# Kernel tuning notes

Measured on AMD Instinct MI355X. Metric: run time of the kernel, lower is better.

Reference implementation:

```python
import jax, jax.numpy as jnp
import numpy as np

B_SZ = 32; CTX = 8192; NP = 512; P = 16          # batch, context, n_patches, patch_size
DM = 1024; DS = 16; DC = 4; EXP = 2               # d_model, d_state, d_conv, expand
DI = EXP * DM                                     # d_inner = 2048
DTR = DM // 16                                    # dt_rank = 64


def _ln(x, g, b, eps=1e-5):
    m = x.mean(-1, keepdims=True)
    v = ((x - m) ** 2).mean(-1, keepdims=True)
    return (x - m) / jnp.sqrt(v + eps) * g + b


def _posemb_sincos_1d(n, d, temperature=10000.0):
    pos = jnp.arange(n, dtype=jnp.float32)
    omega = jnp.arange(d // 2, dtype=jnp.float32) / (d // 2 - 1)
    omega = 1.0 / (temperature ** omega)
    ang = pos[:, None] * omega[None, :]            # [n, d/2]
    return jnp.concatenate([jnp.sin(ang), jnp.cos(ang)], axis=1)  # [n, d]


def setup_inputs() -> dict:
    key = jax.random.key(0)
    ks = jax.random.split(key, 10)
    s = lambda k, shape, scale: jax.random.normal(k, shape, jnp.float32) * scale
    return {
        "x": jax.random.normal(ks[0], (B_SZ, CTX), jnp.float32),
        # patch embedding: LN(patch) -> Linear(P, DM) -> LN(DM)
        "ln1_g": jnp.ones((P,), jnp.float32), "ln1_b": jnp.zeros((P,), jnp.float32),
        "Wp": s(ks[1], (P, DM), P ** -0.5), "bp": jnp.zeros((DM,), jnp.float32),
        "ln2_g": jnp.ones((DM,), jnp.float32), "ln2_b": jnp.zeros((DM,), jnp.float32),
        # Mamba block params (mamba-ssm conventions: in_proj/out_proj bias=False, conv bias=True)
        "W_in": s(ks[2], (DM, 2 * DI), DM ** -0.5),
        "conv_w": s(ks[3], (DI, DC), DC ** -0.5), "conv_b": jnp.zeros((DI,), jnp.float32),
        "W_x": s(ks[4], (DI, DTR + 2 * DS), DI ** -0.5),
        "W_dt": s(ks[5], (DTR, DI), DTR ** -0.5),
        "b_dt": jnp.full((DI,), -4.6, jnp.float32),  # softplus(b_dt) ~ 0.01 (typical dt init)
        "A_log": jnp.log(jnp.broadcast_to(jnp.arange(1, DS + 1, dtype=jnp.float32), (DI, DS))),
        "D": jnp.ones((DI,), jnp.float32),
        "W_out": s(ks[6], (DI, DM), DI ** -0.5),
        "ln3_g": jnp.ones((DM,), jnp.float32), "ln3_b": jnp.zeros((DM,), jnp.float32),
        "Wh": s(ks[7], (DM, 1), DM ** -0.5), "bh": jnp.zeros((1,), jnp.float32),
    }


def reference(x, ln1_g, ln1_b, Wp, bp, ln2_g, ln2_b, W_in, conv_w, conv_b,
              W_x, W_dt, b_dt, A_log, D, W_out, ln3_g, ln3_b, Wh, bh):
    B = x.shape[0]
    # --- patch embedding: 'b 1 (n p) -> b n p' (c=1), LN, Linear, LN ---
    patches = x.reshape(B, NP, P)
    h = _ln(patches, ln1_g, ln1_b)
    h = h @ Wp + bp
    h = _ln(h, ln2_g, ln2_b)                        # [B, NP, DM]
    h = h + _posemb_sincos_1d(NP, DM)
    # --- Mamba block ---
    xz = h @ W_in                                   # [B, NP, 2*DI]
    u, z = jnp.split(xz, 2, axis=-1)                # [B, NP, DI] each
    # causal depthwise conv1d (kernel DC, left-padded), then SiLU
    up = jnp.pad(u, ((0, 0), (DC - 1, 0), (0, 0)))
    uc = sum(up[:, k:k + NP, :] * conv_w[:, k] for k in range(DC)) + conv_b
    uc = jax.nn.silu(uc)
    # input-dependent SSM params
    xd = uc @ W_x                                   # [B, NP, DTR+2*DS]
    dt, Bm, Cm = jnp.split(xd, [DTR, DTR + DS], axis=-1)
    delta = jax.nn.softplus(dt @ W_dt + b_dt)       # [B, NP, DI]
    A = -jnp.exp(A_log)                             # [DI, DS]

    def step(hstate, inps):
        d_t, B_t, C_t, u_t = inps                   # [B,DI], [B,DS], [B,DS], [B,DI]
        dA = jnp.exp(d_t[..., None] * A)            # [B, DI, DS]
        hstate = hstate * dA + (d_t * u_t)[..., None] * B_t[:, None, :]
        y_t = jnp.einsum('bdn,bn->bd', hstate, C_t)
        return hstate, y_t

    h0 = jnp.zeros((B, DI, DS), x.dtype)
    xs = (delta.transpose(1, 0, 2), Bm.transpose(1, 0, 2),
          Cm.transpose(1, 0, 2), uc.transpose(1, 0, 2))
    _, ys = jax.lax.scan(step, h0, xs)              # ys: [NP, B, DI]
    y = ys.transpose(1, 0, 2) + uc * D              # skip connection D*u
    y = y * jax.nn.silu(z)                          # gate
    y = y @ W_out                                   # [B, NP, DM]
    pooled = y.mean(axis=1)                         # [B, DM]
    out = (_ln(pooled, ln3_g, ln3_b) @ Wh + bh).squeeze()  # [B]
    return out
```

## Files before the change

kernel.cpp:

```cpp
#include <hip/hip_runtime.h>
#include <hip/hip_bf16.h>

#define BSZ  32
#define CTX  8192
#define NP_  512
#define PSZ  16
#define DM_  1024
#define DS_  16
#define DI_  2048
#define DTR_ 64
#define NTOK (BSZ*NP_)

typedef __hip_bfloat16 bf16;
typedef short bf16x8 __attribute__((ext_vector_type(8)));
typedef float f32x4  __attribute__((ext_vector_type(4)));

typedef __attribute__((address_space(3))) void lds_t;
typedef __attribute__((address_space(1))) void gbl_t;

__device__ inline float bf2f(bf16 v){ return __bfloat162float(v); }
__device__ inline bf16  f2bf(float v){ return __float2bfloat16(v); }
__device__ inline float bfs2f(short s){ union{unsigned u; float f;} x; x.u = ((unsigned)(unsigned short)s)<<16; return x.f; }
__device__ inline short f2bfs(float v){ bf16 b = f2bf(v); return *reinterpret_cast<short*>(&b); }
__device__ inline float fast_sigmoid(float x){ return 1.0f/(1.0f+__expf(-x)); }
__device__ inline void stout(float* p, float v){ *p = v; }
__device__ inline void stout(bf16* p, float v){ *p = f2bf(v); }
__device__ inline float hw_exp2(float x){ float r; asm("v_exp_f32 %0, %1" : "=v"(r) : "v"(x)); return r; }
__device__ inline float hw_log2(float x){ float r; asm("v_log_f32 %0, %1" : "=v"(r) : "v"(x)); return r; }
__device__ inline float softplus_fast(float x){
  if (x > 15.0f) return x;
  return 0.69314718f * hw_log2(1.0f + hw_exp2(x * 1.44269504f));
}

__device__ inline void gload_lds16(const void* g, void* l){
  __builtin_amdgcn_global_load_lds((const gbl_t*)g, (lds_t*)l, 16, 0, 0);
}

__device__ inline void transpose_cvt_body(
    int bx, int by, const float* __restrict__ W, bf16* __restrict__ T,
    int ldw, int col0, int nvalid, int K, int tid, float (*tile)[65])
{
  int kb = bx << 6, nb = by << 6;
  int c = tid & 63, r4 = tid >> 6;
  #pragma unroll
  for (int i=0;i<16;i++){
    int r = r4 + i*4;
    int kk = kb + r, nn = nb + c;
    float v = 0.f;
    if (kk < K && nn < nvalid) v = W[(size_t)kk*ldw + col0 + nn];
    tile[r][c] = v;
  }
  __syncthreads();
  #pragma unroll
  for (int i=0;i<16;i++){
    int r = r4 + i*4;
    T[(size_t)(nb + r)*K + kb + c] = f2bf(tile[c][r]);
  }
}

__global__ __launch_bounds__(256) void k_prep_all(
    const float* __restrict__ W_in, bf16* __restrict__ winT,
    const float* __restrict__ W_x,  bf16* __restrict__ wxT,
    const float* __restrict__ W_dt, bf16* __restrict__ wdtT,
    float* __restrict__ pe,
    const float* __restrict__ cw, float* __restrict__ cwT)
{
  __shared__ float tile[64][65];
  int b = blockIdx.x, tid = threadIdx.x;
  if (b < 1024){
    transpose_cvt_body(b & 15, b >> 4, W_in, winT, 4096, 0, 4096, 1024, tid, tile);
  } else if (b < 1088){
    int t = b - 1024;
    transpose_cvt_body(t & 31, t >> 5, W_x, wxT, 96, 0, 96, 2048, tid, tile);
  } else if (b < 1120){
    int t = b - 1088;
    transpose_cvt_body(0, t, W_dt, wdtT, 2048, 0, 2048, 64, tid, tile);
  } else if (b < 3168){
    int idx = (b - 1120)*256 + tid;
    int n = idx >> 10, c = idx & 1023;
    int j2 = c & 511;
    float omega = exp2f(-13.2877123795495f * ((float)j2 * (1.0f/511.0f)));
    float ang = (float)n * omega;
    pe[idx] = (c < 512) ? sinf(ang) : cosf(ang);
  } else {
    int idx = (b - 3168)*256 + tid;
    int k = idx >> 11, d = idx & 2047;
    cwT[idx] = cw[d*4 + k];
  }
}

__global__ __launch_bounds__(256) void k_patch(
    const float* __restrict__ x, const float* __restrict__ g1, const float* __restrict__ b1,
    const float* __restrict__ Wp, const float* __restrict__ bp,
    const float* __restrict__ g2, const float* __restrict__ b2,
    const float* __restrict__ pe, bf16* __restrict__ h)
{
  __shared__ float pns[2][16];
  __shared__ float red[8];
  int tid = threadIdx.x;
  int w = tid >> 6, l = tid & 63;
  int tok0 = blockIdx.x << 4;
  int bb = tok0 >> 9, n0 = tok0 & 511;
  float wreg[4][16];
  #pragma unroll
  for (int q=0;q<4;q++)
    #pragma unroll
    for (int i=0;i<16;i++)
      wreg[q][i] = Wp[i*1024 + tid + q*256];
  float bpv[4], g2v[4], b2v[4];
  #pragma unroll
  for (int q=0;q<4;q++){
    int j = tid + q*256;
    bpv[q] = bp[j]; g2v[q] = g2[j]; b2v[q] = b2[j];
  }
  float g1v = 0.f, b1v = 0.f;
  if (tid < 16){ g1v = g1[tid]; b1v = b1[tid]; }
  for (int tt=0; tt<16; ++tt){
    int buf = tt & 1;
    if (tid < 16){
      float v = x[(size_t)bb*CTX + (n0+tt)*16 + tid];
      float m = v;
      #pragma unroll
      for (int o=1;o<16;o<<=1) m += __shfl_xor(m, o, 64);
      m *= (1.0f/16.0f);
      float dv = v - m;
      float s = dv*dv;
      #pragma unroll
      for (int o=1;o<16;o<<=1) s += __shfl_xor(s, o, 64);
      float rs = rsqrtf(s*(1.0f/16.0f) + 1e-5f);
      pns[buf][tid] = dv*rs*g1v + b1v;
    }
    __syncthreads();
    float acc[4];
    #pragma unroll
    for (int q=0;q<4;q++) acc[q] = bpv[q];
    #pragma unroll
    for (int i=0;i<16;i++){
      float p = pns[buf][i];
      #pragma unroll
      for (int q=0;q<4;q++) acc[q] += p*wreg[q][i];
    }
    float s1 = acc[0]+acc[1]+acc[2]+acc[3];
    float s2 = acc[0]*acc[0]+acc[1]*acc[1]+acc[2]*acc[2]+acc[3]*acc[3];
    #pragma unroll
    for (int o=32;o;o>>=1){ s1 += __shfl_down(s1,o,64); s2 += __shfl_down(s2,o,64); }
    if (l==0){ red[w]=s1; red[4+w]=s2; }
    __syncthreads();
    float mu  = (red[0]+red[1]+red[2]+red[3])*(1.0f/1024.0f);
    float var = (red[4]+red[5]+red[6]+red[7])*(1.0f/1024.0f) - mu*mu;
    float rs2 = rsqrtf(var + 1e-5f);
    size_t tok = (size_t)(tok0 + tt);
    #pragma unroll
    for (int q=0;q<4;q++){
      int j = tid + q*256;
      float val = (acc[q]-mu)*rs2*g2v[q] + b2v[q] + pe[(n0+tt)*1024 + j];
      h[tok*1024 + j] = f2bf(val);
    }
  }
}

__global__ __launch_bounds__(512, 2) void k_gemm256(
    const bf16* __restrict__ A, const bf16* __restrict__ BT,
    bf16* __restrict__ Cu, bf16* __restrict__ Cz, int M, int N, int K)
{
  __shared__ __align__(16) bf16 As[2][256*64];
  __shared__ __align__(16) bf16 Bs[2][256*64];
  const int tid = threadIdx.x;
  const int w = tid >> 6, l = tid & 63, lr = l & 15, lg = l >> 4;
  const int wm = w >> 2, wn = w & 3;
  int nblk = N >> 8;
  int nwg = gridDim.x;
  int wg  = (blockIdx.x & 7) * (nwg >> 3) + (blockIdx.x >> 3);
  const int GM = 4;
  int band = GM * nblk;
  int grp = wg / band, loc = wg % band;
  int bm = grp*GM + (loc % GM);
  int bn = loc / GM;
  int m0 = bm << 8, n0 = bn << 8;

  f32x4 acc[8][4] = {};

  int rowS[4], colS[4];
  #pragma unroll
  for (int j=0;j<4;j++){
    int bo = (j*8 + w)*1024 + l*16;
    int r = bo >> 7;
    int c = (bo & 127) ^ ((r & 7) << 4);
    rowS[j] = r; colS[j] = c >> 1;
  }
  const bf16* Ag = A  + (size_t)m0 * K;
  const bf16* Bg = BT + (size_t)n0 * K;

  #define STAGE(buf, kt) do {                                                   \
    _Pragma("unroll")                                                           \
    for (int j=0;j<4;j++)                                                       \
      gload_lds16(Ag + (size_t)rowS[j]*K + (kt) + colS[j], &As[buf][(j*8+w)*512]); \
    _Pragma("unroll")                                                           \
    for (int j=0;j<4;j++)                                                       \
      gload_lds16(Bg + (size_t)rowS[j]*K + (kt) + colS[j], &Bs[buf][(j*8+w)*512]); \
  } while(0)

  int cswz[2];
  cswz[0] = (lg*8) ^ ((lr&7)<<3);
  cswz[1] = (32 + lg*8) ^ ((lr&7)<<3);
  const int rbA = (wm*128 + lr) * 64;
  const int rbB = (wn*64  + lr) * 64;

  #define COMPUTE(buf) do {                                                     \
    _Pragma("unroll")                                                           \
    for (int kk=0;kk<2;kk++){                                                   \
      bf16x8 bq[4];                                                             \
      _Pragma("unroll")                                                         \
      for (int j=0;j<4;j++) bq[j] = *(const bf16x8*)&Bs[buf][rbB + j*1024 + cswz[kk]]; \
      _Pragma("unroll")                                                         \
      for (int rh=0;rh<2;rh++){                                                 \
        bf16x8 af[4];                                                           \
        _Pragma("unroll")                                                       \
        for (int i=0;i<4;i++) af[i] = *(const bf16x8*)&As[buf][rbA + (rh*4+i)*1024 + cswz[kk]]; \
        __builtin_amdgcn_s_setprio(1);                                          \
        _Pragma("unroll")                                                       \
        for (int i=0;i<4;i++)                                                   \
          _Pragma("unroll")                                                     \
          for (int j=0;j<4;j++)                                                 \
            acc[rh*4+i][j] = __builtin_amdgcn_mfma_f32_16x16x32_bf16(af[i], bq[j], acc[rh*4+i][j], 0,0,0); \
        __builtin_amdgcn_s_setprio(0);                                          \
      }                                                                         \
    }                                                                           \
  } while(0)

  STAGE(0, 0);
  STAGE(1, 64);
  const int NT2 = K >> 7;
  int kt = 0;
  for (int t=0; t<NT2; ++t){
    const bool last = (t == NT2-1);
    asm volatile("s_waitcnt vmcnt(8)" ::: "memory");
    __builtin_amdgcn_sched_barrier(0);
    asm volatile("s_barrier" ::: "memory");
    COMPUTE(0);
    asm volatile("s_barrier" ::: "memory");
    __builtin_amdgcn_sched_barrier(0);
    if (!last) STAGE(0, kt + 128);
    if (!last) { asm volatile("s_waitcnt vmcnt(8)" ::: "memory"); }
    else       { asm volatile("s_waitcnt vmcnt(0)" ::: "memory"); }
    __builtin_amdgcn_sched_barrier(0);
    asm volatile("s_barrier" ::: "memory");
    COMPUTE(1);
    if (!last){
      asm volatile("s_barrier" ::: "memory");
      __builtin_amdgcn_sched_barrier(0);
      STAGE(1, kt + 192);
    }
    kt += 128;
  }
  #undef STAGE
  #undef COMPUTE

  #pragma unroll
  for (int fr=0;fr<8;fr++)
    #pragma unroll
    for (int fc=0;fc<4;fc++)
      #pragma unroll
      for (int rr=0;rr<4;rr++){
        int row  = m0 + wm*128 + fr*16 + lg*4 + rr;
        int gcol = n0 + wn*64 + fc*16 + lr;
        float v = acc[fr][fc][rr];
        if (gcol < 2048) Cu[(size_t)row*2048 + gcol] = f2bf(v);
        else { v = v * fast_sigmoid(v); Cz[(size_t)row*2048 + gcol - 2048] = f2bf(v); }
      }
}

template<int EPI, typename OT>
__global__ __launch_bounds__(256) void k_gemm_bt(
    const bf16* __restrict__ A, const bf16* __restrict__ BT, OT* __restrict__ C,
    bf16* __restrict__ C2, int M, int N, int K, const float* __restrict__ bias)
{
  __shared__ __align__(16) bf16 As[128*32];
  __shared__ __align__(16) bf16 Bs[128*32];
  int tid = threadIdx.x;
  int mblk = M >> 7, nblk = N >> 7;
  int nwg = gridDim.x;
  int wg  = (blockIdx.x & 7) * (nwg >> 3) + (blockIdx.x >> 3);
  const int GM = 8;
  int band = GM * nblk;
  int grp = wg / band, loc = wg % band;
  int bm = grp*GM + (loc % GM);
  int bn = loc / GM;
  int m0 = bm << 7, n0 = bn << 7;
  int w = tid >> 6, l = tid & 63, lr = l & 15, lg = l >> 4;
  int wm = w >> 1, wn = w & 1;
  f32x4 acc[4][4] = {};
  int r0 = tid >> 2, c0 = (tid & 3) << 3;
  const bf16* Asrc = A  + (size_t)(m0 + r0) * K + c0;
  const bf16* Bsrc = BT + (size_t)(n0 + r0) * K + c0;
  bf16* AsW = As + w*512;
  bf16* BsW = Bs + w*512;
  for (int kt = 0; kt < K; kt += 32){
    __syncthreads();
    gload_lds16(Asrc + kt,                   AsW);
    gload_lds16(Asrc + (size_t)64*K + kt,    AsW + 2048);
    gload_lds16(Bsrc + kt,                   BsW);
    gload_lds16(Bsrc + (size_t)64*K + kt,    BsW + 2048);
    __syncthreads();
    bf16x8 af[4], bfr[4];
    #pragma unroll
    for (int i=0;i<4;i++) af[i]  = *(const bf16x8*)(As + (wm*64 + i*16 + lr)*32 + lg*8);
    #pragma unroll
    for (int j=0;j<4;j++) bfr[j] = *(const bf16x8*)(Bs + (wn*64 + j*16 + lr)*32 + lg*8);
    #pragma unroll
    for (int i=0;i<4;i++)
      #pragma unroll
      for (int j=0;j<4;j++)
        acc[i][j] = __builtin_amdgcn_mfma_f32_16x16x32_bf16(af[i], bfr[j], acc[i][j], 0,0,0);
  }
  #pragma unroll
  for (int i=0;i<4;i++)
    #pragma unroll
    for (int j=0;j<4;j++)
      #pragma unroll
      for (int r=0;r<4;r++){
        int row = m0 + wm*64 + i*16 + lg*4 + r;
        int col = wn*64 + j*16 + lr;
        int gcol = n0 + col;
        float v = acc[i][j][r];
        if (EPI == 0) stout(&C[(size_t)row*N + gcol], v);
        if (EPI == 1){ v = softplus_fast(v + bias[gcol]); stout(&C[(size_t)row*N + gcol], v); }
      }
}

__global__ __launch_bounds__(256) void k_gemm_xk(
    const bf16* __restrict__ A, const bf16* __restrict__ BT,
    float* __restrict__ C0, float* __restrict__ C1,
    float* __restrict__ C2, float* __restrict__ C3)
{
  __shared__ __align__(16) bf16 As[128*32];
  __shared__ __align__(16) bf16 Bs[128*32];
  int tid = threadIdx.x;
  int nwg = gridDim.x;
  int wg  = (blockIdx.x & 7) * (nwg >> 3) + (blockIdx.x >> 3);
  int chunk = wg >> 7;
  int bm = wg & 127;
  int m0 = bm << 7;
  int kbase = chunk << 9;
  int w = tid >> 6, l = tid & 63, lr = l & 15, lg = l >> 4;
  int wm = w >> 1, wn = w & 1;
  f32x4 acc[4][4] = {};
  int r0 = tid >> 2, c0 = (tid & 3) << 3;
  const bf16* Asrc = A  + (size_t)(m0 + r0) * 2048 + kbase + c0;
  const bf16* Bsrc = BT + (size_t)r0 * 2048 + kbase + c0;
  bf16* AsW = As + w*512;
  bf16* BsW = Bs + w*512;
  float* Cp = (chunk==0) ? C0 : (chunk==1) ? C1 : (chunk==2) ? C2 : C3;
  for (int kt = 0; kt < 512; kt += 32){
    __syncthreads();
    gload_lds16(Asrc + kt,                      AsW);
    gload_lds16(Asrc + (size_t)64*2048 + kt,    AsW + 2048);
    gload_lds16(Bsrc + kt,                      BsW);
    gload_lds16(Bsrc + (size_t)64*2048 + kt,    BsW + 2048);
    __syncthreads();
    bf16x8 af[4], bfr[4];
    #pragma unroll
    for (int i=0;i<4;i++) af[i]  = *(const bf16x8*)(As + (wm*64 + i*16 + lr)*32 + lg*8);
    #pragma unroll
    for (int j=0;j<4;j++) bfr[j] = *(const bf16x8*)(Bs + (wn*64 + j*16 + lr)*32 + lg*8);
    #pragma unroll
    for (int i=0;i<4;i++)
      #pragma unroll
      for (int j=0;j<4;j++)
        acc[i][j] = __builtin_amdgcn_mfma_f32_16x16x32_bf16(af[i], bfr[j], acc[i][j], 0,0,0);
  }
  #pragma unroll
  for (int i=0;i<4;i++)
    #pragma unroll
    for (int j=0;j<4;j++)
      #pragma unroll
      for (int r=0;r<4;r++){
        int row = m0 + wm*64 + i*16 + lg*4 + r;
        int gcol = wn*64 + j*16 + lr;
        Cp[(size_t)row*128 + gcol] = acc[i][j][r];
      }
}

__global__ __launch_bounds__(256) void k_xproj_fix(
    float* __restrict__ xd, const float* __restrict__ p1,
    const float* __restrict__ p2, const float* __restrict__ p3,
    bf16* __restrict__ dt)
{
  int idx = blockIdx.x*256 + threadIdx.x;
  int row = idx >> 7, col = idx & 127;
  float v = xd[idx] + p1[idx] + p2[idx] + p3[idx];
  xd[idx] = v;
  if (col < 64) dt[(row << 6) + col] = f2bf(v);
}

__global__ __launch_bounds__(256) void k_conv(
    const bf16* __restrict__ u, const float* __restrict__ cwT, const float* __restrict__ cb,
    bf16* __restrict__ uc)
{
  int tid = threadIdx.x;
  int d = tid << 3;
  int tok0 = blockIdx.x << 4;
  int n0 = tok0 & 511;
  float wk[4][8];
  #pragma unroll
  for (int k=0;k<4;k++){
    *(float4*)&wk[k][0] = *(const float4*)(cwT + k*2048 + d);
    *(float4*)&wk[k][4] = *(const float4*)(cwT + k*2048 + d + 4);
  }
  float cbv[8];
  *(float4*)&cbv[0] = *(const float4*)(cb + d);
  *(float4*)&cbv[4] = *(const float4*)(cb + d + 4);
  bf16x8 w0, w1, w2;
  if (n0 == 0){
    w0 = (bf16x8){0,0,0,0,0,0,0,0}; w1 = w0; w2 = w0;
  } else {
    w0 = *(const bf16x8*)(u + (size_t)(tok0-3)*2048 + d);
    w1 = *(const bf16x8*)(u + (size_t)(tok0-2)*2048 + d);
    w2 = *(const bf16x8*)(u + (size_t)(tok0-1)*2048 + d);
  }
  #pragma unroll 4
  for (int t=0; t<16; ++t){
    size_t tok = (size_t)(tok0 + t);
    bf16x8 cur = *(const bf16x8*)(u + tok*2048 + d);
    bf16x8 res;
    #pragma unroll
    for (int j=0;j<8;j++){
      float a = cbv[j]
              + wk[0][j]*bfs2f(w0[j]) + wk[1][j]*bfs2f(w1[j])
              + wk[2][j]*bfs2f(w2[j]) + wk[3][j]*bfs2f(cur[j]);
      res[j] = f2bfs(a * fast_sigmoid(a));
    }
    *(bf16x8*)(uc + tok*2048 + d) = res;
    w0 = w1; w1 = w2; w2 = cur;
  }
}

__global__ __launch_bounds__(256) void k_scan(
    const bf16* __restrict__ delta, const bf16* __restrict__ uc, const bf16* __restrict__ g,
    const float* __restrict__ xd, const float* __restrict__ A_log,
    const float* __restrict__ Dp, float* __restrict__ ysum)
{
  __shared__ float red[4][64];
  int tid = threadIdx.x;
  int q = tid >> 6;
  int l = tid & 63;
  int b = blockIdx.x >> 5;
  int d = ((blockIdx.x & 31) << 6) + l;
  const float L2E = 1.44269504f;
  float4 t4 = *(const float4*)(A_log + (size_t)d*16 + q*4);
  float An0 = -__expf(t4.x)*L2E, An1 = -__expf(t4.y)*L2E,
        An2 = -__expf(t4.z)*L2E, An3 = -__expf(t4.w)*L2E;
  float Dd = (q == 0) ? Dp[d] : 0.0f;
  float h0=0.f,h1=0.f,h2=0.f,h3=0.f;
  float acc = 0.0f;
  unsigned o1 = (unsigned)b*1048576u + (unsigned)d;
  unsigned o2 = (unsigned)__builtin_amdgcn_readfirstlane((unsigned)(b*16384 + 16 + q));
  const float4* __restrict__ x4 = (const float4*)xd;
  #pragma unroll 4
  for (int t=0; t<512; ++t){
    float dt = bf2f(delta[o1]);
    float ut = bf2f(uc[o1]);
    float gt = bf2f(g[o1]);
    float4 Bq = x4[o2];
    float4 Cq = x4[o2 + 4u];
    o1 += 2048u; o2 += 32u;
    float du = dt*ut;
    float y;
    float e0 = hw_exp2(dt*An0); h0 = h0*e0 + du*Bq.x; y  = h0*Cq.x;
    float e1 = hw_exp2(dt*An1); h1 = h1*e1 + du*Bq.y; y += h1*Cq.y;
    float e2 = hw_exp2(dt*An2); h2 = h2*e2 + du*Bq.z; y += h2*Cq.z;
    float e3 = hw_exp2(dt*An3); h3 = h3*e3 + du*Bq.w; y += h3*Cq.w;
    acc += (y + ut*Dd) * gt;
  }
  red[q][l] = acc;
  __syncthreads();
  if (q == 0)
    ysum[(size_t)b*2048 + d] = red[0][l] + red[1][l] + red[2][l] + red[3][l];
}

__global__ __launch_bounds__(256) void k_poolgemm_part(
    const float* __restrict__ ysum, const float* __restrict__ Wo, float* __restrict__ partial)
{
  __shared__ float ys[32][64];
  int tid = threadIdx.x;
  int jb = blockIdx.x & 15;
  int kc = blockIdx.x >> 4;
  int j  = jb*64 + (tid & 63);
  int b0 = tid >> 6;
  #pragma unroll
  for (int i=0;i<8;i++){
    int e = tid + i*256;
    int bb = e >> 6, kk = e & 63;
    ys[bb][kk] = ysum[(size_t)bb*2048 + kc*64 + kk];
  }
  __syncthreads();
  float acc[8];
  #pragma unroll
  for (int p=0;p<8;p++) acc[p] = 0.f;
  #pragma unroll 4
  for (int kk=0;kk<64;kk++){
    float wv = Wo[(size_t)(kc*64 + kk)*1024 + j];
    #pragma unroll
    for (int p=0;p<8;p++) acc[p] += ys[b0*8 + p][kk] * wv;
  }
  #pragma unroll
  for (int p=0;p<8;p++)
    partial[((size_t)kc*32 + b0*8 + p)*1024 + j] = acc[p];
}

__global__ __launch_bounds__(256) void k_pool_reduce(
    const float* __restrict__ partial, float* __restrict__ pooled)
{
  int idx = blockIdx.x*256 + threadIdx.x;
  float s = 0.f;
  #pragma unroll 8
  for (int kc=0;kc<32;kc++) s += partial[(size_t)kc*32768 + idx];
  pooled[idx] = s * (1.0f/512.0f);
}

__global__ __launch_bounds__(256) void k_head(
    const float* __restrict__ pooled, const float* __restrict__ g, const float* __restrict__ bb,
    const float* __restrict__ Wh, const float* __restrict__ bh, float* __restrict__ out)
{
  __shared__ float red[8];
  int b = blockIdx.x, tid = threadIdx.x;
  float v[4];
  #pragma unroll
  for (int q=0;q<4;q++) v[q] = pooled[(size_t)b*1024 + tid + q*256];
  float s1 = v[0]+v[1]+v[2]+v[3];
  float s2 = v[0]*v[0]+v[1]*v[1]+v[2]*v[2]+v[3]*v[3];
  #pragma unroll
  for (int o=32;o;o>>=1){ s1 += __shfl_down(s1,o,64); s2 += __shfl_down(s2,o,64); }
  int w = tid>>6, l = tid&63;
  if (l==0){ red[w]=s1; red[4+w]=s2; }
  __syncthreads();
  float mu  = (red[0]+red[1]+red[2]+red[3])*(1.0f/1024.0f);
  float var = (red[4]+red[5]+red[6]+red[7])*(1.0f/1024.0f) - mu*mu;
  float rs = rsqrtf(var + 1e-5f);
  float p = 0.f;
  #pragma unroll
  for (int q=0;q<4;q++){
    int jv = tid + q*256;
    p += ((v[q]-mu)*rs*g[jv] + bb[jv]) * Wh[jv];
  }
  #pragma unroll
  for (int o=32;o;o>>=1) p += __shfl_down(p,o,64);
  __syncthreads();
  if (l==0) red[w] = p;
  __syncthreads();
  if (tid==0) out[b] = red[0]+red[1]+red[2]+red[3] + bh[0];
}

extern "C" void kernel_launch(void* const* d_in, const int* in_sizes, int n_in,
                              void* d_out, int out_size, void* d_ws, size_t ws_size,
                              hipStream_t stream)
{
  const float* x     = (const float*)d_in[0];
  const float* ln1_g = (const float*)d_in[1];
  const float* ln1_b = (const float*)d_in[2];
  const float* Wp    = (const float*)d_in[3];
  const float* bp    = (const float*)d_in[4];
  const float* ln2_g = (const float*)d_in[5];
  const float* ln2_b = (const float*)d_in[6];
  const float* W_in  = (const float*)d_in[7];
  const float* conv_w= (const float*)d_in[8];
  const float* conv_b= (const float*)d_in[9];
  const float* W_x   = (const float*)d_in[10];
  const float* W_dt  = (const float*)d_in[11];
  const float* b_dt  = (const float*)d_in[12];
  const float* A_log = (const float*)d_in[13];
  const float* Dv    = (const float*)d_in[14];
  const float* W_out = (const float*)d_in[15];
  const float* ln3_g = (const float*)d_in[16];
  const float* ln3_b = (const float*)d_in[17];
  const float* Wh    = (const float*)d_in[18];
  const float* bh    = (const float*)d_in[19];

  char* ws = (char*)d_ws;
  size_t o = 0;
  bf16*  u_delta = (bf16*)(ws + o); o += (size_t)NTOK*DI_*2;
  bf16*  zbuf    = (bf16*)(ws + o); o += (size_t)NTOK*DI_*2;
  bf16*  ucbuf   = (bf16*)(ws + o); o += (size_t)NTOK*DI_*2;
  char*  poolA   = (ws + o);        o += (size_t)NTOK*DM_*2;
  bf16*  winT    = (bf16*)(ws + o); o += (size_t)2*DI_*DM_*2;
  float* pe      = (float*)(ws + o); o += (size_t)NP_*DM_*4;
  bf16*  wxT     = (bf16*)(ws + o); o += (size_t)128*2048*2;
  bf16*  wdtT    = (bf16*)(ws + o); o += (size_t)2048*64*2;
  float* cwT     = (float*)(ws + o); o += (size_t)4*2048*4;
  bf16*  hbuf    = (bf16*)poolA;
  float* xdbuf   = (float*)(poolA + 0);
  bf16*  dtbuf   = (bf16*) (poolA + 8388608);
  float* ysumbuf = (float*)(poolA + 11272192);
  float* pooledb = (float*)(poolA + 11534336);
  float* partial = (float*)(poolA + 12582912);
  float* xpart1  = (float*)winT;
  float* xpart2  = (float*)u_delta;
  float* xpart3  = (float*)((char*)u_delta + 8388608);

  k_prep_all      <<<3200, 256, 0, stream>>>(W_in, winT, W_x, wxT, W_dt, wdtT, pe, conv_w, cwT);
  k_patch         <<<1024, 256, 0, stream>>>(x, ln1_g, ln1_b, Wp, bp, ln2_g, ln2_b, pe, hbuf);
  k_gemm256       <<<1024, 512, 0, stream>>>(hbuf, winT, u_delta, zbuf, NTOK, 4096, 1024);
  k_conv          <<<1024, 256, 0, stream>>>(u_delta, cwT, conv_b, ucbuf);
  k_gemm_xk       <<<512,  256, 0, stream>>>(ucbuf, wxT, xdbuf, xpart1, xpart2, xpart3);
  k_xproj_fix     <<<8192, 256, 0, stream>>>(xdbuf, xpart1, xpart2, xpart3, dtbuf);
  k_gemm_bt<1,bf16><<<2048,256, 0, stream>>>(dtbuf, wdtT, u_delta, nullptr, NTOK, 2048, 64, b_dt);
  k_scan          <<<1024, 256, 0, stream>>>(u_delta, ucbuf, zbuf, xdbuf, A_log, Dv, ysumbuf);
  k_poolgemm_part <<<512,  256, 0, stream>>>(ysumbuf, W_out, partial);
  k_pool_reduce   <<<128,  256, 0, stream>>>(partial, pooledb);
  k_head          <<<32,   256, 0, stream>>>(pooledb, ln3_g, ln3_b, Wh, bh, (float*)d_out);
  (void)in_sizes; (void)n_in; (void)out_size; (void)ws_size;
}
```

Before: 438.0 us.

## Retile in_proj GEMM to 128x256 blocks with 256 threads and K=32 stages

The in_proj GEMM moves from a 256x256 tile with 512 threads and 64-wide K stages to a 128x256 tile with 256 threads (4 waves, each 64x128) and 32-wide K stages. The grid doubles to 2048 workgroups. The LDS swizzle, staging offsets, vmcnt waits and epilogue indexing are rewritten to match. The smaller LDS footprint and thread count are meant to raise occupancy and scheduling flexibility, at the cost of less data reuse per tile, more barriers per unit of K, and more global traffic for the B operand.

```diff
diff --git a/kernel.cpp b/kernel.cpp
--- a/kernel.cpp
+++ b/kernel.cpp
@@ -159,15 +159,15 @@
   }
 }
 
-__global__ __launch_bounds__(512, 2) void k_gemm256(
+__global__ __launch_bounds__(256, 2) void k_gemm256(
     const bf16* __restrict__ A, const bf16* __restrict__ BT,
     bf16* __restrict__ Cu, bf16* __restrict__ Cz, int M, int N, int K)
 {
-  __shared__ __align__(16) bf16 As[2][256*64];
-  __shared__ __align__(16) bf16 Bs[2][256*64];
+  __shared__ __align__(16) bf16 As[2][128*32];
+  __shared__ __align__(16) bf16 Bs[2][256*32];
   const int tid = threadIdx.x;
   const int w = tid >> 6, l = tid & 63, lr = l & 15, lg = l >> 4;
-  const int wm = w >> 2, wn = w & 3;
+  const int wm = w >> 1, wn = w & 1;
   int nblk = N >> 8;
   int nwg = gridDim.x;
   int wg  = (blockIdx.x & 7) * (nwg >> 3) + (blockIdx.x >> 3);
@@ -176,72 +176,70 @@
   int grp = wg / band, loc = wg % band;
   int bm = grp*GM + (loc % GM);
   int bn = loc / GM;
-  int m0 = bm << 8, n0 = bn << 8;
-
-  f32x4 acc[8][4] = {};
-
-  int rowS[4], colS[4];
+  int m0 = bm << 7, n0 = bn << 8;
+
+  f32x4 acc[4][8] = {};
+
+  int rowA[2], colA[2], rowB[4], colB[4];
+  #pragma unroll
+  for (int j=0;j<2;j++){
+    int bo = j*4096 + w*1024 + l*16;
+    int r = bo >> 6;
+    int c = (bo & 63) ^ ((r & 3) << 4);
+    rowA[j] = r; colA[j] = c >> 1;
+  }
   #pragma unroll
   for (int j=0;j<4;j++){
-    int bo = (j*8 + w)*1024 + l*16;
-    int r = bo >> 7;
-    int c = (bo & 127) ^ ((r & 7) << 4);
-    rowS[j] = r; colS[j] = c >> 1;
+    int bo = j*4096 + w*1024 + l*16;
+    int r = bo >> 6;
+    int c = (bo & 63) ^ ((r & 3) << 4);
+    rowB[j] = r; colB[j] = c >> 1;
   }
   const bf16* Ag = A  + (size_t)m0 * K;
   const bf16* Bg = BT + (size_t)n0 * K;
 
   #define STAGE(buf, kt) do {                                                   \
     _Pragma("unroll")                                                           \
-    for (int j=0;j<4;j++)                                                       \
-      gload_lds16(Ag + (size_t)rowS[j]*K + (kt) + colS[j], &As[buf][(j*8+w)*512]); \
+    for (int j=0;j<2;j++)                                                       \
+      gload_lds16(Ag + (size_t)rowA[j]*K + (kt) + colA[j], &As[buf][j*2048 + w*512]); \
     _Pragma("unroll")                                                           \
     for (int j=0;j<4;j++)                                                       \
-      gload_lds16(Bg + (size_t)rowS[j]*K + (kt) + colS[j], &Bs[buf][(j*8+w)*512]); \
+      gload_lds16(Bg + (size_t)rowB[j]*K + (kt) + colB[j], &Bs[buf][j*2048 + w*512]); \
   } while(0)
 
-  int cswz[2];
-  cswz[0] = (lg*8) ^ ((lr&7)<<3);
-  cswz[1] = (32 + lg*8) ^ ((lr&7)<<3);
-  const int rbA = (wm*128 + lr) * 64;
-  const int rbB = (wn*64  + lr) * 64;
+  const int cswz = (lg*8) ^ ((lr&3)<<3);
+  const int rbA = (wm*64  + lr) * 32;
+  const int rbB = (wn*128 + lr) * 32;
 
   #define COMPUTE(buf) do {                                                     \
+    bf16x8 bq[8];                                                               \
     _Pragma("unroll")                                                           \
-    for (int kk=0;kk<2;kk++){                                                   \
-      bf16x8 bq[4];                                                             \
+    for (int j=0;j<8;j++) bq[j] = *(const bf16x8*)&Bs[buf][rbB + j*512 + cswz]; \
+    __builtin_amdgcn_s_setprio(1);                                              \
+    _Pragma("unroll")                                                           \
+    for (int i=0;i<4;i++){                                                      \
+      bf16x8 af = *(const bf16x8*)&As[buf][rbA + i*512 + cswz];                 \
       _Pragma("unroll")                                                         \
-      for (int j=0;j<4;j++) bq[j] = *(const bf16x8*)&Bs[buf][rbB + j*1024 + cswz[kk]]; \
-      _Pragma("unroll")                                                         \
-      for (int rh=0;rh<2;rh++){                                                 \
-        bf16x8 af[4];                                                           \
-        _Pragma("unroll")                                                       \
-        for (int i=0;i<4;i++) af[i] = *(const bf16x8*)&As[buf][rbA + (rh*4+i)*1024 + cswz[kk]]; \
-        __builtin_amdgcn_s_setprio(1);                                          \
-        _Pragma("unroll")                                                       \
-        for (int i=0;i<4;i++)                                                   \
-          _Pragma("unroll")                                                     \
-          for (int j=0;j<4;j++)                                                 \
-            acc[rh*4+i][j] = __builtin_amdgcn_mfma_f32_16x16x32_bf16(af[i], bq[j], acc[rh*4+i][j], 0,0,0); \
-        __builtin_amdgcn_s_setprio(0);                                          \
-      }                                                                         \
+      for (int j=0;j<8;j++)                                                     \
+        acc[i][j] = __builtin_amdgcn_mfma_f32_16x16x32_bf16(af, bq[j], acc[i][j], 0,0,0); \
     }                                                                           \
+    __builtin_amdgcn_s_setprio(0);                                              \
   } while(0)
 
   STAGE(0, 0);
-  STAGE(1, 64);
-  const int NT2 = K >> 7;
+  STAGE(1, 32);
+  const int NT2 = K >> 6;
   int kt = 0;
   for (int t=0; t<NT2; ++t){
     const bool last = (t == NT2-1);
-    asm volatile("s_waitcnt vmcnt(8)" ::: "memory");
+    asm volatile("s_waitcnt vmcnt(6)" ::: "memory");
     __builtin_amdgcn_sched_barrier(0);
     asm volatile("s_barrier" ::: "memory");
     COMPUTE(0);
     asm volatile("s_barrier" ::: "memory");
     __builtin_amdgcn_sched_barrier(0);
-    if (!last) STAGE(0, kt + 128);
-    if (!last) { asm volatile("s_waitcnt vmcnt(8)" ::: "memory"); }
+    if (!last) STAGE(0, kt + 64);
+    if (!last) { asm volatile("s_waitcnt vmcnt(6)" ::: "memory"); }
     else       { asm volatile("s_waitcnt vmcnt(0)" ::: "memory"); }
     __builtin_amdgcn_sched_barrier(0);
     asm volatile("s_barrier" ::: "memory");
@@ -249,22 +247,22 @@
     if (!last){
       asm volatile("s_barrier" ::: "memory");
       __builtin_amdgcn_sched_barrier(0);
-      STAGE(1, kt + 192);
+      STAGE(1, kt + 96);
     }
-    kt += 128;
+    kt += 64;
   }
   #undef STAGE
   #undef COMPUTE
 
   #pragma unroll
-  for (int fr=0;fr<8;fr++)
-    #pragma unroll
-    for (int fc=0;fc<4;fc++)
+  for (int i=0;i<4;i++)
+    #pragma unroll
+    for (int j=0;j<8;j++)
       #pragma unroll
       for (int rr=0;rr<4;rr++){
-        int row  = m0 + wm*128 + fr*16 + lg*4 + rr;
-        int gcol = n0 + wn*64 + fc*16 + lr;
-        float v = acc[fr][fc][rr];
+        int row  = m0 + wm*64 + i*16 + lg*4 + rr;
+        int gcol = n0 + wn*128 + j*16 + lr;
+        float v = acc[i][j][rr];
         if (gcol < 2048) Cu[(size_t)row*2048 + gcol] = f2bf(v);
         else { v = v * fast_sigmoid(v); Cz[(size_t)row*2048 + gcol - 2048] = f2bf(v); }
       }
@@ -599,7 +597,7 @@
 
   k_prep_all      <<<3200, 256, 0, stream>>>(W_in, winT, W_x, wxT, W_dt, wdtT, pe, conv_w, cwT);
   k_patch         <<<1024, 256, 0, stream>>>(x, ln1_g, ln1_b, Wp, bp, ln2_g, ln2_b, pe, hbuf);
-  k_gemm256       <<<1024, 512, 0, stream>>>(hbuf, winT, u_delta, zbuf, NTOK, 4096, 1024);
+  k_gemm256       <<<2048, 256, 0, stream>>>(hbuf, winT, u_delta, zbuf, NTOK, 4096, 1024);
   k_conv          <<<1024, 256, 0, stream>>>(u_delta, cwT, conv_b, ucbuf);
   k_gemm_xk       <<<512,  256, 0, stream>>>(ucbuf, wxT, xdbuf, xpart1, xpart2, xpart3);
   k_xproj_fix     <<<8192, 256, 0, stream>>>(xdbuf, xpart1, xpart2, xpart3, dtbuf);
```

Measured after the change: 457.8 us. +4.5%, slower.
